# Kernel tuning notes

Hardware: AMD Instinct MI355X
Metric: run time of the kernel (lower is better)

Reference implementation:

```python
import jax, jax.numpy as jnp
import numpy as np

B, M, W, C, NN, J, ED, EMB = 8, 4096, 128, 32, 16, 4, 5, 2
EPS = 1e-5


def setup_inputs() -> dict:
    key = jax.random.key(0)
    ks = jax.random.split(key, 30)
    s = 0.05
    x = jax.random.normal(ks[0], (B, M, W), jnp.float32)
    pseudo = jax.random.normal(ks[1], (M * NN, EMB), jnp.float32)
    # structured indices: row r scatters its NN attention weights into row r of the m x m matrix
    nbr = jax.random.randint(ks[2], (M, NN), 0, M)
    L_idx = (jnp.arange(M)[:, None] * M + nbr).reshape(-1).astype(jnp.int32)
    inp = dict(x=x, pseudo=pseudo, L_idx=L_idx)
    inp['edge_w'] = jax.random.normal(ks[3], (ED, EMB), jnp.float32) * s
    inp['edge_b'] = jnp.zeros((ED,), jnp.float32)
    # Gaussian mixture params per layer (J components, encode_dim each); reset_parameters -> N(0,1)
    inp['mu0'] = jax.random.normal(ks[4], (J, ED), jnp.float32)
    inp['sigma0'] = jax.random.normal(ks[5], (J, ED), jnp.float32)
    inp['mu1'] = jax.random.normal(ks[6], (J, ED), jnp.float32)
    inp['sigma1'] = jax.random.normal(ks[7], (J, ED), jnp.float32)
    # layer 0: W -> C ; layer 1: C -> C
    inp['l1w0'] = jax.random.normal(ks[8], (C, W), jnp.float32) * s
    inp['l1b0'] = jnp.zeros((C,), jnp.float32)
    inp['l2w0'] = jax.random.normal(ks[9], (C, W), jnp.float32) * s
    inp['l2b0'] = jnp.zeros((C,), jnp.float32)
    inp['l1w1'] = jax.random.normal(ks[10], (C, C), jnp.float32) * s
    inp['l1b1'] = jnp.zeros((C,), jnp.float32)
    inp['l2w1'] = jax.random.normal(ks[11], (C, C), jnp.float32) * s
    inp['l2b1'] = jnp.zeros((C,), jnp.float32)
    inp['bn_g0'] = jnp.ones((C,), jnp.float32)
    inp['bn_b0'] = jnp.zeros((C,), jnp.float32)
    inp['bn_g1'] = jnp.ones((C,), jnp.float32)
    inp['bn_b1'] = jnp.zeros((C,), jnp.float32)
    inp['fc1w'] = jax.random.normal(ks[12], (256, M * C), jnp.float32) * 0.005
    inp['fc1b'] = jnp.zeros((256,), jnp.float32)
    inp['fc2w'] = jax.random.normal(ks[13], (53, 256), jnp.float32) * s
    inp['fc2b'] = jnp.zeros((53,), jnp.float32)
    return inp


def _get_L(pseudo, L_idx, edge_w, edge_b, mu, sigma, dtype):
    # Gaussian-mixture edge attention: u^T diag(sigma) u per component, summed, exp(-0.5 *)
    emb = pseudo @ edge_w.T + edge_b                      # (E, ED), E = M*NN
    u = emb[None, :, :] - mu[:, None, :]                  # (J, E, ED)
    q = jnp.sum(u * u * sigma[:, None, :], axis=-1)       # (J, E)
    w = jnp.sum(jnp.exp(-0.5 * q), axis=0)                # (E,)
    attn = jax.nn.softmax(w.reshape(M, NN), axis=1).reshape(-1)
    return jnp.zeros(M * M, dtype).at[L_idx].set(attn).reshape(M, M)


def _layer(x, L, w1, b1, w2, b2, g, bb):
    Lx = jnp.einsum('mn,bnf->bmf', L, x)                  # graph conv
    h = Lx @ w1.T + b1 + x @ w2.T + b2                    # (B, M, C)
    # BatchNorm1d (training mode): stats over batch and node dims, biased variance
    mean = jnp.mean(h, axis=(0, 1))
    var = jnp.var(h, axis=(0, 1))
    h = (h - mean) * jax.lax.rsqrt(var + EPS) * g + bb
    return jax.nn.relu(h)


def reference(x, pseudo, L_idx, edge_w, edge_b, mu0, sigma0, mu1, sigma1,
              l1w0, l1b0, l2w0, l2b0, l1w1, l1b1, l2w1, l2b1,
              bn_g0, bn_b0, bn_g1, bn_b1, fc1w, fc1b, fc2w, fc2b):
    L0 = _get_L(pseudo, L_idx, edge_w, edge_b, mu0, sigma0, x.dtype)
    h = _layer(x, L0, l1w0, l1b0, l2w0, l2b0, bn_g0, bn_b0)
    L1 = _get_L(pseudo, L_idx, edge_w, edge_b, mu1, sigma1, x.dtype)
    h = _layer(h, L1, l1w1, l1b1, l2w1, l2b1, bn_g1, bn_b1)
    flat = h.reshape(B, M * C)
    out = jax.nn.relu(flat @ fc1w.T + fc1b)               # dropout = identity (eval)
    return out @ fc2w.T + fc2b                            # (B, 53)
```

## Files before the change

### kernel.cpp

```cpp
#include <hip/hip_runtime.h>

#define B_ 8
#define M_ 4096
#define W_ 128
#define C_ 32
#define NN_ 16

typedef short s16x8 __attribute__((ext_vector_type(8)));
typedef float f32x4 __attribute__((ext_vector_type(4)));

static __device__ __forceinline__ unsigned short f2bf(float f) {
  unsigned u = __builtin_bit_cast(unsigned, f);
  u = u + 0x7FFFu + ((u >> 16) & 1u);
  return (unsigned short)(u >> 16);
}
static __device__ __forceinline__ s16x8 cvt8v(float4 a, float4 b) {
  s16x8 r;
  r[0] = (short)f2bf(a.x); r[1] = (short)f2bf(a.y);
  r[2] = (short)f2bf(a.z); r[3] = (short)f2bf(a.w);
  r[4] = (short)f2bf(b.x); r[5] = (short)f2bf(b.y);
  r[6] = (short)f2bf(b.z); r[7] = (short)f2bf(b.w);
  return r;
}
static __device__ __forceinline__ float safeexp(float a) {
  return expf(fminf(a, 87.f));
}

__global__ void poison_kernel(float* __restrict__ out, int n, float val) {
  int t = blockIdx.x * blockDim.x + threadIdx.x;
  if (t < n) out[t] = val;
}

__global__ __launch_bounds__(256) void init_kernel(
    float* __restrict__ fc1acc, const float* __restrict__ fc1b,
    float* __restrict__ bn) {
  int g = blockIdx.x * 256 + threadIdx.x;
  if (g < 2048) fc1acc[g] = fc1b[g & 255];
  else if (g < 34816) bn[g - 2048] = 0.f;
}

__global__ __launch_bounds__(256) void attn_kernel(
    const float* __restrict__ pseudo, const int* __restrict__ Lidx,
    const float* __restrict__ edge_w, const float* __restrict__ edge_b,
    const float* __restrict__ mu0, const float* __restrict__ sg0,
    const float* __restrict__ mu1, const float* __restrict__ sg1,
    float* __restrict__ we0, float* __restrict__ we1, int* __restrict__ colb) {
  int m = blockIdx.x * 256 + threadIdx.x;
  if (m >= M_) return;
  float w0[NN_], w1[NN_];
  int col[NN_];
#pragma unroll
  for (int n = 0; n < NN_; n++) {
    int e = m * NN_ + n;
    float p0 = pseudo[e * 2], p1 = pseudo[e * 2 + 1];
    float emb[5];
#pragma unroll
    for (int d = 0; d < 5; d++)
      emb[d] = p0 * edge_w[d * 2] + p1 * edge_w[d * 2 + 1] + edge_b[d];
    float a0 = 0.f, a1 = 0.f;
#pragma unroll
    for (int j = 0; j < 4; j++) {
      float qa = 0.f, qb = 0.f;
#pragma unroll
      for (int d = 0; d < 5; d++) {
        float u0 = emb[d] - mu0[j * 5 + d];
        qa += u0 * u0 * sg0[j * 5 + d];
        float u1 = emb[d] - mu1[j * 5 + d];
        qb += u1 * u1 * sg1[j * 5 + d];
      }
      a0 += safeexp(-0.5f * qa);
      a1 += safeexp(-0.5f * qb);
    }
    w0[n] = a0; w1[n] = a1;
    col[n] = Lidx[e] % M_;
  }
  float mx0 = w0[0], mx1 = w1[0];
#pragma unroll
  for (int n = 1; n < NN_; n++) { mx0 = fmaxf(mx0, w0[n]); mx1 = fmaxf(mx1, w1[n]); }
  float s0 = 0.f, s1 = 0.f;
#pragma unroll
  for (int n = 0; n < NN_; n++) {
    w0[n] = safeexp(w0[n] - mx0); s0 += w0[n];
    w1[n] = safeexp(w1[n] - mx1); s1 += w1[n];
  }
  float r0 = 1.f / s0, r1 = 1.f / s1;
#pragma unroll
  for (int n = 0; n < NN_; n++) {
    bool last = true;
#pragma unroll
    for (int n2 = n + 1; n2 < NN_; n2++)
      if (col[n2] == col[n]) last = false;
    int e = m * NN_ + n;
    we0[e] = last ? w0[n] * r0 : 0.f;
    we1[e] = last ? w1[n] * r1 : 0.f;
    colb[e] = col[n];
  }
}

__global__ __launch_bounds__(256) void proj0_kernel(
    const float* __restrict__ x, const float* __restrict__ l1w0,
    const float* __restrict__ l2w0, float* __restrict__ G) {
  int lane = threadIdx.x & 63, wave = threadIdx.x >> 6;
  int l16 = lane & 15, quad = lane >> 4;
  int tile = blockIdx.x * 4 + wave;
  s16x8 bf[4][4];
#pragma unroll
  for (int kit = 0; kit < 4; kit++) {
#pragma unroll
    for (int ct = 0; ct < 4; ct++) {
      int out = ct * 16 + l16;
      const float* src = (out < 32 ? l1w0 + out * 128 : l2w0 + (out - 32) * 128)
                         + kit * 32 + quad * 8;
      bf[kit][ct] = cvt8v(*(const float4*)src, *(const float4*)(src + 4));
    }
  }
  f32x4 acc[4];
#pragma unroll
  for (int ct = 0; ct < 4; ct++) acc[ct] = (f32x4){0.f, 0.f, 0.f, 0.f};
  int row = tile * 16 + l16;
  const float* xr = x + (size_t)row * 128 + quad * 8;
#pragma unroll
  for (int kit = 0; kit < 4; kit++) {
    const float* ap = xr + kit * 32;
    s16x8 a = cvt8v(*(const float4*)ap, *(const float4*)(ap + 4));
#pragma unroll
    for (int ct = 0; ct < 4; ct++)
      acc[ct] = __builtin_amdgcn_mfma_f32_16x16x32_bf16(a, bf[kit][ct], acc[ct], 0, 0, 0);
  }
  int rbase = tile * 16 + quad * 4;
#pragma unroll
  for (int ct = 0; ct < 4; ct++)
#pragma unroll
    for (int i = 0; i < 4; i++)
      G[(size_t)(rbase + i) * 64 + ct * 16 + l16] = acc[ct][i];
}

__global__ __launch_bounds__(256) void conv_kernel(
    const float* __restrict__ G,
    const float* __restrict__ we, const int* __restrict__ colb,
    const float* __restrict__ b1c, const float* __restrict__ b2c,
    float* __restrict__ h, float* __restrict__ bns, float* __restrict__ bnq) {
  __shared__ float s_we[8][16];
  __shared__ int   s_cn[8][16];
  __shared__ float s_s[32], s_q[32];
  int tid = threadIdx.x;
  if (tid < 128) {
    int row = tid >> 4, nn = tid & 15;
    int m = (blockIdx.x * 8 + row) & 4095;
    s_we[row][nn] = we[m * 16 + nn];
    s_cn[row][nn] = colb[m * 16 + nn];
  } else if (tid < 160) {
    s_s[tid - 128] = 0.f;
    s_q[tid - 128] = 0.f;
  }
  __syncthreads();
  int row = tid >> 5, c = tid & 31;
  int r = blockIdx.x * 8 + row;
  int b = r >> 12;
  const float* Gb = G + ((size_t)b << 18);
  float acc = 0.f;
#pragma unroll
  for (int nn = 0; nn < NN_; nn++)
    acc += s_we[row][nn] * Gb[s_cn[row][nn] * 64 + c];
  float hv = acc + G[(size_t)r * 64 + 32 + c] + b1c[c] + b2c[c];
  h[(size_t)r * 32 + c] = hv;
  atomicAdd(&s_s[c], hv);
  atomicAdd(&s_q[c], hv * hv);
  __syncthreads();
  if (tid < 32) {
    int slot = blockIdx.x & 255;
    atomicAdd(&bns[tid * 256 + slot], s_s[tid]);
    atomicAdd(&bnq[tid * 256 + slot], s_q[tid]);
  }
}

__global__ void bnfin_kernel(const float* __restrict__ bns, const float* __restrict__ bnq,
                             const float* __restrict__ g, const float* __restrict__ bb,
                             float* __restrict__ scale, float* __restrict__ shift) {
  int c = threadIdx.x;
  if (c >= 32) return;
  float s = 0.f, q = 0.f;
  for (int i = 0; i < 256; i++) { s += bns[c * 256 + i]; q += bnq[c * 256 + i]; }
  float mean = s * (1.f / 32768.f);
  float var = fmaxf(q * (1.f / 32768.f) - mean * mean, 0.f);
  float sc = g[c] * rsqrtf(var + 1e-5f);
  scale[c] = sc;
  shift[c] = bb[c] - mean * sc;
}

__global__ __launch_bounds__(256) void proj1_kernel(
    const float* __restrict__ h0, const float* __restrict__ sc0,
    const float* __restrict__ l1w1, const float* __restrict__ l2w1,
    float* __restrict__ G) {
  int lane = threadIdx.x & 63, wave = threadIdx.x >> 6;
  int l16 = lane & 15, quad = lane >> 4;
  int tile = blockIdx.x * 4 + wave;
  s16x8 bf[4];
#pragma unroll
  for (int ct = 0; ct < 4; ct++) {
    int out = ct * 16 + l16;
    const float* src = (out < 32 ? l1w1 + out * 32 : l2w1 + (out - 32) * 32) + quad * 8;
    bf[ct] = cvt8v(*(const float4*)src, *(const float4*)(src + 4));
  }
  float scv[8], shv[8];
#pragma unroll
  for (int j = 0; j < 8; j++) {
    scv[j] = sc0[quad * 8 + j];
    shv[j] = sc0[32 + quad * 8 + j];
  }
  int row = tile * 16 + l16;
  const float* hr = h0 + (size_t)row * 32 + quad * 8;
  float4 hv0 = *(const float4*)hr;
  float4 hv1 = *(const float4*)(hr + 4);
  float av[8] = {hv0.x, hv0.y, hv0.z, hv0.w, hv1.x, hv1.y, hv1.z, hv1.w};
  s16x8 a;
#pragma unroll
  for (int j = 0; j < 8; j++)
    a[j] = (short)f2bf(fmaxf(av[j] * scv[j] + shv[j], 0.f));
  f32x4 acc[4];
#pragma unroll
  for (int ct = 0; ct < 4; ct++) {
    f32x4 z = {0.f, 0.f, 0.f, 0.f};
    acc[ct] = __builtin_amdgcn_mfma_f32_16x16x32_bf16(a, bf[ct], z, 0, 0, 0);
  }
  int rbase = tile * 16 + quad * 4;
#pragma unroll
  for (int ct = 0; ct < 4; ct++)
#pragma unroll
    for (int i = 0; i < 4; i++)
      G[(size_t)(rbase + i) * 64 + ct * 16 + l16] = acc[ct][i];
}

__global__ __launch_bounds__(256, 4) void fc1_kernel(
    const float* __restrict__ h1, const float* __restrict__ sc1,
    const float* __restrict__ fc1w, float* __restrict__ fc1acc) {
  __shared__ float a1s[8][1024];
  int kc = blockIdx.x >> 3;
  int og = blockIdx.x & 7;
  int kbase = kc << 10;
  int obase = og << 5;
  for (int idx = threadIdx.x; idx < 8192; idx += 256) {
    int b = idx >> 10, k = idx & 1023;
    int c = k & 31;
    a1s[b][k] = fmaxf(h1[((size_t)b << 17) + kbase + k] * sc1[c] + sc1[32 + c], 0.f);
  }
  __syncthreads();
  int lane = threadIdx.x & 63, wave = threadIdx.x >> 6;
  float acc[8][8];
#pragma unroll
  for (int i = 0; i < 8; i++)
#pragma unroll
    for (int b = 0; b < 8; b++) acc[i][b] = 0.f;
#pragma unroll
  for (int it = 0; it < 4; it++) {
    float4 h4[8];
#pragma unroll
    for (int b = 0; b < 8; b++) h4[b] = *(const float4*)&a1s[b][it * 256 + lane * 4];
#pragma unroll
    for (int i = 0; i < 8; i++) {
      int o = obase + wave * 8 + i;
      const float* wp = fc1w + (size_t)o * 131072 + kbase + it * 256 + lane * 4;
      float4 w4 = *(const float4*)wp;
#pragma unroll
      for (int b = 0; b < 8; b++)
        acc[i][b] += w4.x * h4[b].x + w4.y * h4[b].y + w4.z * h4[b].z + w4.w * h4[b].w;
    }
  }
  float myval = 0.f;
#pragma unroll
  for (int i = 0; i < 8; i++) {
#pragma unroll
    for (int b = 0; b < 8; b++) {
      float v = acc[i][b];
#pragma unroll
      for (int off = 1; off < 64; off <<= 1) v += __shfl_xor(v, off);
      if (lane == i * 8 + b) myval = v;
    }
  }
  atomicAdd(&fc1acc[(lane & 7) * 256 + obase + wave * 8 + (lane >> 3)], myval);
}

__global__ void fc2_kernel(const float* __restrict__ fc1acc,
                           const float* __restrict__ fc2w,
                           const float* __restrict__ fc2b,
                           float* __restrict__ out) {
  int t = blockIdx.x * blockDim.x + threadIdx.x;
  if (t >= 424) return;
  int b = t / 53, j = t - b * 53;
  float s = fc2b[j];
  const float* fa = fc1acc + b * 256;
  const float* wr = fc2w + j * 256;
#pragma unroll 8
  for (int o = 0; o < 256; o++) s += fmaxf(fa[o], 0.f) * wr[o];
  out[t] = s;
}

extern "C" void kernel_launch(void* const* d_in, const int* in_sizes, int n_in,
                              void* d_out, int out_size, void* d_ws, size_t ws_size,
                              hipStream_t stream) {
  float* out = (float*)d_out;
  int bad = 0;
  if (n_in != 25) bad = 2;
  else if (in_sizes[0] != 4194304) bad = 3;
  else if (in_sizes[2] != 65536) bad = 4;
  else if (in_sizes[21] != 33554432) bad = 5;
  else if (out_size != 424) bad = 6;
  else if (ws_size < 13509120) bad = 1;
  if (bad) {
    poison_kernel<<<2, 256, 0, stream>>>(out, out_size, (float)bad * 1.0e6f);
    return;
  }

  const float* x      = (const float*)d_in[0];
  const float* pseudo = (const float*)d_in[1];
  const int*   Lidx   = (const int*)d_in[2];
  const float* edge_w = (const float*)d_in[3];
  const float* edge_b = (const float*)d_in[4];
  const float* mu0    = (const float*)d_in[5];
  const float* sg0    = (const float*)d_in[6];
  const float* mu1    = (const float*)d_in[7];
  const float* sg1    = (const float*)d_in[8];
  const float* l1w0   = (const float*)d_in[9];
  const float* l1b0   = (const float*)d_in[10];
  const float* l2w0   = (const float*)d_in[11];
  const float* l2b0   = (const float*)d_in[12];
  const float* l1w1   = (const float*)d_in[13];
  const float* l1b1   = (const float*)d_in[14];
  const float* l2w1   = (const float*)d_in[15];
  const float* l2b1   = (const float*)d_in[16];
  const float* bng0   = (const float*)d_in[17];
  const float* bnb0   = (const float*)d_in[18];
  const float* bng1   = (const float*)d_in[19];
  const float* bnb1   = (const float*)d_in[20];
  const float* fc1w   = (const float*)d_in[21];
  const float* fc1b   = (const float*)d_in[22];
  const float* fc2w   = (const float*)d_in[23];
  const float* fc2b   = (const float*)d_in[24];

  char* Wp = (char*)d_ws;
  int*   colb   = (int*)  (Wp + 0);
  float* we0    = (float*)(Wp + 262144);
  float* we1    = (float*)(Wp + 524288);
  float* G      = (float*)(Wp + 786432);
  float* h0     = (float*)(Wp + 9175040);
  float* h1     = (float*)(Wp + 9175040);
  float* bn     = (float*)(Wp + 13369344);
  float* sc     = (float*)(Wp + 13500416);
  float* fc1acc = (float*)(Wp + 13500928);

  init_kernel<<<136, 256, 0, stream>>>(fc1acc, fc1b, bn);
  attn_kernel<<<16, 256, 0, stream>>>(pseudo, Lidx, edge_w, edge_b,
                                      mu0, sg0, mu1, sg1, we0, we1, colb);
  proj0_kernel<<<512, 256, 0, stream>>>(x, l1w0, l2w0, G);
  conv_kernel<<<4096, 256, 0, stream>>>(G, we0, colb, l1b0, l2b0,
                                        h0, bn, bn + 8192);
  bnfin_kernel<<<1, 32, 0, stream>>>(bn, bn + 8192, bng0, bnb0, sc, sc + 32);
  proj1_kernel<<<512, 256, 0, stream>>>(h0, sc, l1w1, l2w1, G);
  conv_kernel<<<4096, 256, 0, stream>>>(G, we1, colb, l1b1, l2b1,
                                        h1, bn + 16384, bn + 24576);
  bnfin_kernel<<<1, 32, 0, stream>>>(bn + 16384, bn + 24576, bng1, bnb1,
                                     sc + 64, sc + 96);
  fc1_kernel<<<1024, 256, 0, stream>>>(h1, sc + 64, fc1w, fc1acc);
  fc2_kernel<<<2, 256, 0, stream>>>(fc1acc, fc2w, fc2b, out);
}
```

Baseline: 390.8 us.

## Move fc1 GEMV onto bf16 MFMA with swizzled LDS, parallelize BN finalize

fc1 now stages normalized activations as bf16 in XOR-swizzled shared memory, padded to 16 rows with the 8 unused rows zeroed. It converts fc1w rows to bf16 on the fly and accumulates with 16x16x32 MFMA instead of scalar FMAs followed by wave shuffle reductions. The grid is halved and each block now covers 64 outputs. bnfin spreads its 256-element reduction across 256 threads and combines the partials in shared memory instead of looping serially in 32 threads. The cost is bf16 rounding of the 134M-element fc1 weight and activation product, plus half of the MFMA output rows wasted on padding.

```diff
diff --git a/kernel.cpp b/kernel.cpp
--- a/kernel.cpp
+++ b/kernel.cpp
@@ -174,18 +174,32 @@
   }
 }
 
-__global__ void bnfin_kernel(const float* __restrict__ bns, const float* __restrict__ bnq,
-                             const float* __restrict__ g, const float* __restrict__ bb,
-                             float* __restrict__ scale, float* __restrict__ shift) {
-  int c = threadIdx.x;
-  if (c >= 32) return;
+__global__ __launch_bounds__(256) void bnfin_kernel(
+    const float* __restrict__ bns, const float* __restrict__ bnq,
+    const float* __restrict__ g, const float* __restrict__ bb,
+    float* __restrict__ scale, float* __restrict__ shift) {
+  __shared__ float red[2][8][32];
+  int tid = threadIdx.x;
+  int c = tid & 31, part = tid >> 5;
   float s = 0.f, q = 0.f;
-  for (int i = 0; i < 256; i++) { s += bns[c * 256 + i]; q += bnq[c * 256 + i]; }
-  float mean = s * (1.f / 32768.f);
-  float var = fmaxf(q * (1.f / 32768.f) - mean * mean, 0.f);
-  float sc = g[c] * rsqrtf(var + 1e-5f);
-  scale[c] = sc;
-  shift[c] = bb[c] - mean * sc;
+#pragma unroll 8
+  for (int i = 0; i < 32; i++) {
+    s += bns[c * 256 + part * 32 + i];
+    q += bnq[c * 256 + part * 32 + i];
+  }
+  red[0][part][c] = s;
+  red[1][part][c] = q;
+  __syncthreads();
+  if (tid < 32) {
+    float S = 0.f, Q = 0.f;
+#pragma unroll
+    for (int p = 0; p < 8; p++) { S += red[0][p][tid]; Q += red[1][p][tid]; }
+    float mean = S * (1.f / 32768.f);
+    float var = fmaxf(Q * (1.f / 32768.f) - mean * mean, 0.f);
+    float sc = g[tid] * rsqrtf(var + 1e-5f);
+    scale[tid] = sc;
+    shift[tid] = bb[tid] - mean * sc;
+  }
 }
 
 __global__ __launch_bounds__(256) void proj1_kernel(
@@ -231,53 +245,52 @@
       G[(size_t)(rbase + i) * 64 + ct * 16 + l16] = acc[ct][i];
 }
 
-__global__ __launch_bounds__(256, 4) void fc1_kernel(
+__global__ __launch_bounds__(256) void fc1_kernel(
     const float* __restrict__ h1, const float* __restrict__ sc1,
     const float* __restrict__ fc1w, float* __restrict__ fc1acc) {
-  __shared__ float a1s[8][1024];
-  int kc = blockIdx.x >> 3;
-  int og = blockIdx.x & 7;
-  int kbase = kc << 10;
-  int obase = og << 5;
-  for (int idx = threadIdx.x; idx < 8192; idx += 256) {
-    int b = idx >> 10, k = idx & 1023;
-    int c = k & 31;
-    a1s[b][k] = fmaxf(h1[((size_t)b << 17) + kbase + k] * sc1[c] + sc1[32 + c], 0.f);
+  __shared__ short als[16 * 1024];
+  int tid = threadIdx.x;
+  int kc = blockIdx.x >> 2;
+  int og = blockIdx.x & 3;
+  size_t kbase = (size_t)kc << 10;
+  for (int s = tid; s < 4096; s += 256) {
+    int rowb = s >> 8;
+    int k4 = (s & 255) << 2;
+    short4 v4 = {0, 0, 0, 0};
+    if (rowb < 8) {
+      float4 hv = *(const float4*)(h1 + ((size_t)rowb << 17) + kbase + k4);
+      int c = k4 & 31;
+      float4 scv = *(const float4*)(sc1 + c);
+      float4 shv = *(const float4*)(sc1 + 32 + c);
+      v4.x = (short)f2bf(fmaxf(hv.x * scv.x + shv.x, 0.f));
+      v4.y = (short)f2bf(fmaxf(hv.y * scv.y + shv.y, 0.f));
+      v4.z = (short)f2bf(fmaxf(hv.z * scv.z + shv.z, 0.f));
+      v4.w = (short)f2bf(fmaxf(hv.w * scv.w + shv.w, 0.f));
+    }
+    int byte = ((rowb << 11) + (k4 << 1)) ^ ((rowb & 7) << 4);
+    *(short4*)((char*)als + byte) = v4;
   }
   __syncthreads();
-  int lane = threadIdx.x & 63, wave = threadIdx.x >> 6;
-  float acc[8][8];
-#pragma unroll
-  for (int i = 0; i < 8; i++)
-#pragma unroll
-    for (int b = 0; b < 8; b++) acc[i][b] = 0.f;
-#pragma unroll
-  for (int it = 0; it < 4; it++) {
-    float4 h4[8];
-#pragma unroll
-    for (int b = 0; b < 8; b++) h4[b] = *(const float4*)&a1s[b][it * 256 + lane * 4];
-#pragma unroll
-    for (int i = 0; i < 8; i++) {
-      int o = obase + wave * 8 + i;
-      const float* wp = fc1w + (size_t)o * 131072 + kbase + it * 256 + lane * 4;
-      float4 w4 = *(const float4*)wp;
-#pragma unroll
-      for (int b = 0; b < 8; b++)
-        acc[i][b] += w4.x * h4[b].x + w4.y * h4[b].y + w4.z * h4[b].z + w4.w * h4[b].w;
-    }
-  }
-  float myval = 0.f;
-#pragma unroll
-  for (int i = 0; i < 8; i++) {
-#pragma unroll
-    for (int b = 0; b < 8; b++) {
-      float v = acc[i][b];
-#pragma unroll
-      for (int off = 1; off < 64; off <<= 1) v += __shfl_xor(v, off);
-      if (lane == i * 8 + b) myval = v;
-    }
-  }
-  atomicAdd(&fc1acc[(lane & 7) * 256 + obase + wave * 8 + (lane >> 3)], myval);
+  int lane = tid & 63, wave = tid >> 6;
+  int l16 = lane & 15, quad = lane >> 4;
+  const float* wrow = fc1w + (size_t)(og * 64 + wave * 16 + l16) * 131072
+                      + kbase + quad * 8;
+  int abase = (l16 << 11) + (quad << 4);
+  int axor = (l16 & 7) << 4;
+  f32x4 acc = {0.f, 0.f, 0.f, 0.f};
+#pragma unroll 4
+  for (int kk = 0; kk < 32; kk++) {
+    const float* wp = wrow + kk * 32;
+    s16x8 bfr = cvt8v(*(const float4*)wp, *(const float4*)(wp + 4));
+    s16x8 afr = *(const s16x8*)((const char*)als + ((abase + (kk << 6)) ^ axor));
+    acc = __builtin_amdgcn_mfma_f32_16x16x32_bf16(afr, bfr, acc, 0, 0, 0);
+  }
+  if (quad < 2) {
+    int o = og * 64 + wave * 16 + l16;
+#pragma unroll
+    for (int i = 0; i < 4; i++)
+      atomicAdd(&fc1acc[(quad * 4 + i) * 256 + o], acc[i]);
+  }
 }
 
 __global__ void fc2_kernel(const float* __restrict__ fc1acc,
@@ -354,12 +367,12 @@
   proj0_kernel<<<512, 256, 0, stream>>>(x, l1w0, l2w0, G);
   conv_kernel<<<4096, 256, 0, stream>>>(G, we0, colb, l1b0, l2b0,
                                         h0, bn, bn + 8192);
-  bnfin_kernel<<<1, 32, 0, stream>>>(bn, bn + 8192, bng0, bnb0, sc, sc + 32);
+  bnfin_kernel<<<1, 256, 0, stream>>>(bn, bn + 8192, bng0, bnb0, sc, sc + 32);
   proj1_kernel<<<512, 256, 0, stream>>>(h0, sc, l1w1, l2w1, G);
   conv_kernel<<<4096, 256, 0, stream>>>(G, we1, colb, l1b1, l2b1,
                                         h1, bn + 16384, bn + 24576);
-  bnfin_kernel<<<1, 32, 0, stream>>>(bn + 16384, bn + 24576, bng1, bnb1,
-                                     sc + 64, sc + 96);
-  fc1_kernel<<<1024, 256, 0, stream>>>(h1, sc + 64, fc1w, fc1acc);
+  bnfin_kernel<<<1, 256, 0, stream>>>(bn + 16384, bn + 24576, bng1, bnb1,
+                                      sc + 64, sc + 96);
+  fc1_kernel<<<512, 256, 0, stream>>>(h1, sc + 64, fc1w, fc1acc);
   fc2_kernel<<<2, 256, 0, stream>>>(fc1acc, fc2w, fc2b, out);
 }
```

Result: faster. 346.5 us (-11.3%).
